# Performance work log

Measured on AMD Instinct MI355X. Metric: run time of the kernel, lower is better.

The kernel has to match this reference:

```python
import jax, jax.numpy as jnp
import numpy as np

B, C, OUT, K, H, W = 16, 128, 128, 3, 128, 128
EPS = 1e-5


def setup_inputs() -> dict:
    key = jax.random.key(0)
    ks = jax.random.split(key, 16)
    s = 0.05  # weight init scale to keep activations tame
    d = {
        "ir_feat": jax.random.normal(ks[0], (B, C, H, W), jnp.float32),
        "vi_feat": jax.random.normal(ks[1], (B, C, H, W), jnp.float32),
        # kernel_gen: 1x1 convs on pooled [B,2C,1,1] -> matmuls
        "kg_w1": jax.random.normal(ks[2], (C // 2, 2 * C), jnp.float32) * s,
        "kg_b1": jax.random.normal(ks[3], (C // 2,), jnp.float32) * s,
        "kg_w2": jax.random.normal(ks[4], (OUT * C * K * K, C // 2), jnp.float32) * s,
        "kg_b2": jax.random.normal(ks[5], (OUT * C * K * K,), jnp.float32) * s,
        # bias_gen
        "bg_w1": jax.random.normal(ks[6], (C // 4, 2 * C), jnp.float32) * s,
        "bg_b1": jax.random.normal(ks[7], (C // 4,), jnp.float32) * s,
        "bg_w2": jax.random.normal(ks[8], (OUT, C // 4), jnp.float32) * s,
        "bg_b2": jax.random.normal(ks[9], (OUT,), jnp.float32) * s,
        # enhance: 1x1 conv (no bias) + BN (eval-mode running stats)
        "en_w": jax.random.normal(ks[10], (C, 2 * C), jnp.float32) * s,
        "bn_gamma": jnp.ones((C,), jnp.float32),
        "bn_beta": jnp.zeros((C,), jnp.float32),
        "bn_mean": jax.random.normal(ks[11], (C,), jnp.float32) * 0.1,
        "bn_var": jax.random.uniform(ks[12], (C,), jnp.float32, 0.5, 1.5),
    }
    return d


def reference(ir_feat, vi_feat, kg_w1, kg_b1, kg_w2, kg_b2,
              bg_w1, bg_b1, bg_w2, bg_b2, en_w,
              bn_gamma, bn_beta, bn_mean, bn_var):
    concat = jnp.concatenate([ir_feat, vi_feat], axis=1)        # [B,2C,H,W]
    pooled = concat.mean(axis=(2, 3))                            # AdaptiveAvgPool2d(1) -> [B,2C]

    # dynamic kernel generation (1x1 convs on 1x1 spatial == matmuls)
    hk = jax.nn.relu(pooled @ kg_w1.T + kg_b1)                   # [B,C/2]
    dyn_k = (hk @ kg_w2.T + kg_b2).reshape(B, OUT, C, K, K)      # per-sample conv weights
    hb = jax.nn.relu(pooled @ bg_w1.T + bg_b1)                   # [B,C/4]
    dyn_b = hb @ bg_w2.T + bg_b2                                 # [B,OUT]

    # enhance: 1x1 conv -> BN(eval) -> ReLU
    enh = jnp.einsum('bchw,oc->bohw', concat, en_w)              # [B,C,H,W]
    inv = (bn_gamma / jnp.sqrt(bn_var + EPS))[:, None, None]
    enh = jax.nn.relu(enh * inv + (bn_beta - bn_mean * bn_gamma / jnp.sqrt(bn_var + EPS))[:, None, None])

    # per-sample dynamic conv2d, batched via vmap (replaces the python loop)
    def conv_one(x, w, b):  # x:[C,H,W], w:[OUT,C,K,K], b:[OUT]
        y = jax.lax.conv_general_dilated(
            x[None], w, window_strides=(1, 1), padding=[(1, 1), (1, 1)],
            dimension_numbers=('NCHW', 'OIHW', 'NCHW'))[0]
        return y + b[:, None, None]

    return jax.vmap(conv_one)(enh, dyn_k, dyn_b)                 # [B,OUT,H,W]
```

## Files before the change

### kernel.cpp

```cpp
#include <hip/hip_runtime.h>
#include <hip/hip_bf16.h>

#define B_    16
#define C_    128
#define TWOC  256
#define OUT_  128
#define HW    16384
#define WDIM  128
#define HDIM  128
#define KTOT  1152

typedef __attribute__((ext_vector_type(8))) short short8;
typedef __attribute__((ext_vector_type(4))) float floatx4;

__device__ __forceinline__ ushort f2bf(float f) {
    union { float f; uint u; } x; x.f = f;
    uint r = (x.u + 0x7FFFu + ((x.u >> 16) & 1u)) >> 16;
    return (ushort)r;
}
__device__ __forceinline__ float bf2f(ushort u) {
    union { float f; uint u; } x; x.u = ((uint)u) << 16;
    return x.f;
}

__global__ __launch_bounds__(256) void zero_pooled_kernel(float* __restrict__ p) {
    int i = blockIdx.x * 256 + threadIdx.x;
    if (i < B_ * TWOC) p[i] = 0.f;
}

__global__ __launch_bounds__(256) void enhance_kernel(
    const float* __restrict__ ir, const float* __restrict__ vi,
    const float* __restrict__ en_w,
    const float* __restrict__ gamma, const float* __restrict__ beta,
    const float* __restrict__ mean, const float* __restrict__ var,
    ushort* __restrict__ enh, float* __restrict__ pooled)
{
    __shared__ ushort Xs[128][40];
    __shared__ float red[256];
    int b = blockIdx.y;
    int p0 = blockIdx.x * 128;
    int t = threadIdx.x;
    int lane = t & 63, wave = t >> 6;
    int wr = wave >> 1, wc = wave & 1;
    int lr = lane & 15, kg = lane >> 4;
    int px = t & 127, half = t >> 7;

    floatx4 acc[4][4] = {};
    float pp[8];

    #pragma unroll
    for (int kc = 0; kc < 8; ++kc) {
        int c2b = kc * 32 + half * 16;
        const float* src = (c2b < C_) ? (ir + ((size_t)b * C_ + c2b) * HW + p0 + px)
                                      : (vi + ((size_t)b * C_ + (c2b - C_)) * HW + p0 + px);
        uint u[8];
        #pragma unroll
        for (int jj = 0; jj < 8; ++jj) {
            float f0 = src[(size_t)(2 * jj) * HW];
            float f1 = src[(size_t)(2 * jj + 1) * HW];
            u[jj] = (uint)f2bf(f0) | ((uint)f2bf(f1) << 16);
        }
        __syncthreads();
        uint4* dst = (uint4*)&Xs[px][half * 16];
        dst[0] = make_uint4(u[0], u[1], u[2], u[3]);
        dst[1] = make_uint4(u[4], u[5], u[6], u[7]);
        __syncthreads();

        short8 af[4], bfr[4];
        #pragma unroll
        for (int i2 = 0; i2 < 4; ++i2) {
            int co = wr * 64 + i2 * 16 + lr;
            const float* wp = en_w + (size_t)co * TWOC + kc * 32 + kg * 8;
            float4 w0 = *(const float4*)wp;
            float4 w1 = *(const float4*)(wp + 4);
            short8 a;
            a[0] = (short)f2bf(w0.x); a[1] = (short)f2bf(w0.y);
            a[2] = (short)f2bf(w0.z); a[3] = (short)f2bf(w0.w);
            a[4] = (short)f2bf(w1.x); a[5] = (short)f2bf(w1.y);
            a[6] = (short)f2bf(w1.z); a[7] = (short)f2bf(w1.w);
            af[i2] = a;
        }
        #pragma unroll
        for (int j = 0; j < 4; ++j) {
            int pl = wc * 64 + j * 16 + lr;
            bfr[j] = *(const short8*)&Xs[pl][kg * 8];
        }
        #pragma unroll
        for (int i2 = 0; i2 < 4; ++i2)
            #pragma unroll
            for (int j = 0; j < 4; ++j)
                acc[i2][j] = __builtin_amdgcn_mfma_f32_16x16x32_bf16(af[i2], bfr[j], acc[i2][j], 0, 0, 0);

        {
            int c = t & 31, grp = t >> 5;
            float s = 0.f;
            #pragma unroll
            for (int q = 0; q < 16; ++q) s += bf2f(Xs[grp * 16 + q][c]);
            pp[kc] = s;
        }
    }

    #pragma unroll
    for (int i2 = 0; i2 < 4; ++i2) {
        int co_b = wr * 64 + i2 * 16 + kg * 4;
        float4 g  = *(const float4*)&gamma[co_b];
        float4 vv = *(const float4*)&var[co_b];
        float4 bt = *(const float4*)&beta[co_b];
        float4 mn = *(const float4*)&mean[co_b];
        float inv0 = g.x * rsqrtf(vv.x + 1e-5f), inv1 = g.y * rsqrtf(vv.y + 1e-5f);
        float inv2 = g.z * rsqrtf(vv.z + 1e-5f), inv3 = g.w * rsqrtf(vv.w + 1e-5f);
        float ad0 = bt.x - mn.x * inv0, ad1 = bt.y - mn.y * inv1;
        float ad2 = bt.z - mn.z * inv2, ad3 = bt.w - mn.w * inv3;
        #pragma unroll
        for (int j = 0; j < 4; ++j) {
            int pl = wc * 64 + j * 16 + lr;
            float v0 = fmaxf(acc[i2][j][0] * inv0 + ad0, 0.f);
            float v1 = fmaxf(acc[i2][j][1] * inv1 + ad1, 0.f);
            float v2 = fmaxf(acc[i2][j][2] * inv2 + ad2, 0.f);
            float v3 = fmaxf(acc[i2][j][3] * inv3 + ad3, 0.f);
            uint2 pk;
            pk.x = (uint)f2bf(v0) | ((uint)f2bf(v1) << 16);
            pk.y = (uint)f2bf(v2) | ((uint)f2bf(v3) << 16);
            *(uint2*)&enh[((size_t)b * HW + p0 + pl) * C_ + co_b] = pk;
        }
    }

    #pragma unroll
    for (int kc = 0; kc < 8; ++kc) {
        __syncthreads();
        red[t] = pp[kc];
        __syncthreads();
        if (t < 32) {
            float s = red[t] + red[32 + t] + red[64 + t] + red[96 + t]
                    + red[128 + t] + red[160 + t] + red[192 + t] + red[224 + t];
            atomicAdd(&pooled[b * TWOC + kc * 32 + t], s);
        }
    }
}

__global__ __launch_bounds__(256) void gen_mlp1_kernel(
    const float* __restrict__ pooled,
    const float* __restrict__ kg_w1, const float* __restrict__ kg_b1,
    const float* __restrict__ bg_w1, const float* __restrict__ bg_b1,
    float* __restrict__ hk, float* __restrict__ hb)
{
    const float scale = 1.0f / (float)HW;
    int idx = blockIdx.x * 256 + threadIdx.x;
    if (idx < B_ * 64) {
        int b = idx >> 6, j = idx & 63;
        const float4* w = (const float4*)(kg_w1 + (size_t)j * TWOC);
        const float4* p = (const float4*)(pooled + b * TWOC);
        float s = 0.f;
        #pragma unroll 8
        for (int q = 0; q < 64; ++q) {
            float4 wv = w[q], pv = p[q];
            s += (wv.x * pv.x + wv.y * pv.y) + (wv.z * pv.z + wv.w * pv.w);
        }
        hk[idx] = fmaxf(kg_b1[j] + s * scale, 0.f);
    } else if (idx < B_ * 64 + B_ * 32) {
        int e = idx - B_ * 64;
        int b = e >> 5, j = e & 31;
        const float4* w = (const float4*)(bg_w1 + (size_t)j * TWOC);
        const float4* p = (const float4*)(pooled + b * TWOC);
        float s = 0.f;
        #pragma unroll 8
        for (int q = 0; q < 64; ++q) {
            float4 wv = w[q], pv = p[q];
            s += (wv.x * pv.x + wv.y * pv.y) + (wv.z * pv.z + wv.w * pv.w);
        }
        hb[e] = fmaxf(bg_b1[j] + s * scale, 0.f);
    }
}

__global__ __launch_bounds__(256) void gen_dynk_kernel(
    const float* __restrict__ kg_w2, const float* __restrict__ kg_b2,
    const float* __restrict__ hk, const float* __restrict__ hb,
    const float* __restrict__ bg_w2, const float* __restrict__ bg_b2,
    ushort* __restrict__ dynk, float* __restrict__ dyn_b)
{
    __shared__ float hk_s[B_][64];
    int t = threadIdx.x;
    for (int i = t; i < B_ * 64; i += 256) hk_s[i >> 6][i & 63] = hk[i];
    __syncthreads();

    int i = blockIdx.x * 256 + t;
    int kk = i >> 14;
    int o  = (i >> 7) & 127;
    int c  = i & 127;
    int r  = o * KTOT + c * 9 + kk;

    float wrow[64];
    const float4* w4 = (const float4*)(kg_w2 + (size_t)r * 64);
    #pragma unroll
    for (int q = 0; q < 16; ++q) {
        float4 v = w4[q];
        wrow[4 * q + 0] = v.x; wrow[4 * q + 1] = v.y;
        wrow[4 * q + 2] = v.z; wrow[4 * q + 3] = v.w;
    }
    float bias = kg_b2[r];
    #pragma unroll
    for (int b = 0; b < B_; ++b) {
        float s = bias;
        #pragma unroll
        for (int k2 = 0; k2 < 64; ++k2) s += hk_s[b][k2] * wrow[k2];
        dynk[((size_t)(b * 9 + kk) * 128 + o) * 128 + c] = f2bf(s);
    }

    if (blockIdx.x == 0) {
        for (int e = t; e < B_ * OUT_; e += 256) {
            int b = e >> 7, o2 = e & 127;
            float s = bg_b2[o2];
            const float* w = bg_w2 + o2 * 32;
            const float* h = hb + b * 32;
            #pragma unroll
            for (int k2 = 0; k2 < 32; ++k2) s += h[k2] * w[k2];
            dyn_b[e] = s;
        }
    }
}

__global__ __launch_bounds__(256, 3) void dynconv_kernel(
    const ushort* __restrict__ enh, const ushort* __restrict__ dynk,
    const float* __restrict__ dyn_b, float* __restrict__ out)
{
    __shared__ ushort halo[180][72];
    const int b = blockIdx.z;
    const int gy0 = blockIdx.y * 8, gx0 = blockIdx.x * 16;
    const int t = threadIdx.x, lane = t & 63, wave = t >> 6;
    const int wr = wave >> 1, wc = wave & 1;
    const int lr = lane & 15, kg = lane >> 4;
    const ushort* dynk_b = dynk + (size_t)b * 9 * 128 * 128;
    const ushort* enh_b  = enh + (size_t)b * HW * C_;

    floatx4 acc[4][4] = {};
    short8 a_cur[8], a_nxt[8];

    for (int h = 0; h < 2; ++h) {
        uint4 hreg[6];
        #pragma unroll
        for (int s = 0; s < 6; ++s) {
            int seg = s * 256 + t;
            int hp = seg >> 3, c8 = seg & 7;
            uint4 v = make_uint4(0, 0, 0, 0);
            if (hp < 180) {
                int hy = hp / 18, hx = hp - hy * 18;
                int gy = gy0 - 1 + hy, gx = gx0 - 1 + hx;
                if ((unsigned)gy < 128u && (unsigned)gx < 128u)
                    v = *(const uint4*)&enh_b[((size_t)(gy * WDIM + gx)) * C_ + h * 64 + c8 * 8];
            }
            hreg[s] = v;
        }
        #pragma unroll
        for (int q = 0; q < 8; ++q) {
            int ks = q >> 2, i2 = q & 3;
            int o = wr * 64 + i2 * 16 + lr;
            a_cur[q] = *(const short8*)&dynk_b[(size_t)(0 * 128 + o) * 128 + h * 64 + ks * 32 + kg * 8];
        }
        __syncthreads();
        #pragma unroll
        for (int s = 0; s < 6; ++s) {
            int seg = s * 256 + t;
            int hp = seg >> 3, c8 = seg & 7;
            if (hp < 180) *(uint4*)&halo[hp][c8 * 8] = hreg[s];
        }
        __syncthreads();

        #pragma unroll
        for (int kk = 0; kk < 9; ++kk) {
            if (kk < 8) {
                #pragma unroll
                for (int q = 0; q < 8; ++q) {
                    int ks = q >> 2, i2 = q & 3;
                    int o = wr * 64 + i2 * 16 + lr;
                    a_nxt[q] = *(const short8*)&dynk_b[(size_t)((kk + 1) * 128 + o) * 128 + h * 64 + ks * 32 + kg * 8];
                }
            }
            const int kh = kk / 3, kw = kk - kh * 3;
            #pragma unroll
            for (int ks = 0; ks < 2; ++ks) {
                short8 bfr[4];
                #pragma unroll
                for (int j = 0; j < 4; ++j) {
                    int p = wc * 64 + j * 16 + lr;
                    int py = p >> 4, px = p & 15;
                    bfr[j] = *(const short8*)&halo[(py + kh) * 18 + (px + kw)][ks * 32 + kg * 8];
                }
                #pragma unroll
                for (int i2 = 0; i2 < 4; ++i2)
                    #pragma unroll
                    for (int j = 0; j < 4; ++j)
                        acc[i2][j] = __builtin_amdgcn_mfma_f32_16x16x32_bf16(a_cur[ks * 4 + i2], bfr[j], acc[i2][j], 0, 0, 0);
            }
            #pragma unroll
            for (int q = 0; q < 8; ++q) a_cur[q] = a_nxt[q];
        }
    }

    #pragma unroll
    for (int i2 = 0; i2 < 4; ++i2) {
        int o_b = wr * 64 + i2 * 16 + kg * 4;
        float4 db = *(const float4*)&dyn_b[b * OUT_ + o_b];
        float dbv[4] = {db.x, db.y, db.z, db.w};
        #pragma unroll
        for (int j = 0; j < 4; ++j) {
            int p = wc * 64 + j * 16 + lr;
            int py = p >> 4, px = p & 15;
            int gy = gy0 + py, gx = gx0 + px;
            #pragma unroll
            for (int r = 0; r < 4; ++r) {
                int o = o_b + r;
                out[((size_t)(b * OUT_ + o)) * HW + gy * WDIM + gx] = acc[i2][j][r] + dbv[r];
            }
        }
    }
}

extern "C" void kernel_launch(void* const* d_in, const int* in_sizes, int n_in,
                              void* d_out, int out_size, void* d_ws, size_t ws_size,
                              hipStream_t stream)
{
    const float* ir    = (const float*)d_in[0];
    const float* vi    = (const float*)d_in[1];
    const float* kg_w1 = (const float*)d_in[2];
    const float* kg_b1 = (const float*)d_in[3];
    const float* kg_w2 = (const float*)d_in[4];
    const float* kg_b2 = (const float*)d_in[5];
    const float* bg_w1 = (const float*)d_in[6];
    const float* bg_b1 = (const float*)d_in[7];
    const float* bg_w2 = (const float*)d_in[8];
    const float* bg_b2 = (const float*)d_in[9];
    const float* en_w  = (const float*)d_in[10];
    const float* bn_g  = (const float*)d_in[11];
    const float* bn_b  = (const float*)d_in[12];
    const float* bn_m  = (const float*)d_in[13];
    const float* bn_v  = (const float*)d_in[14];
    float* out = (float*)d_out;

    char* ws = (char*)d_ws;
    float*  pooled = (float*)(ws + 0);
    float*  dyn_b  = (float*)(ws + 16384);
    float*  hk     = (float*)(ws + 24576);
    float*  hb     = (float*)(ws + 28672);
    ushort* dynk   = (ushort*)(ws + 32768);
    ushort* enh    = (ushort*)(ws + 32768 + 4718592);

    zero_pooled_kernel<<<16, 256, 0, stream>>>(pooled);
    enhance_kernel<<<dim3(HDIM, B_), 256, 0, stream>>>(ir, vi, en_w, bn_g, bn_b,
                                                       bn_m, bn_v, enh, pooled);
    gen_mlp1_kernel<<<6, 256, 0, stream>>>(pooled, kg_w1, kg_b1, bg_w1, bg_b1, hk, hb);
    gen_dynk_kernel<<<576, 256, 0, stream>>>(kg_w2, kg_b2, hk, hb, bg_w2, bg_b2, dynk, dyn_b);
    dynconv_kernel<<<dim3(WDIM / 16, HDIM / 8, B_), 256, 0, stream>>>(enh, dynk, dyn_b, out);
}
```

Baseline: 694.3 us.

## Prefetch next channel chunk in enhance kernel and pre-convert weights to bf16

The enhance kernel now loads the next chunk of input channels and weights into registers while the current chunk runs its MFMAs, a software-pipelining scheme. A new prep kernel converts en_w to bf16 once and replaces the zero kernel. The pooled reduction is interleaved into the main loop instead of running as a separate tail loop. Packed bf16 conversion uses the v_cvt_pk_bf16_f32 instruction. This raises register pressure, and when the workspace is too small the bf16 weights are parked in the tail of the output buffer, which later gets overwritten by the final kernel.

```diff
diff --git a/kernel.cpp b/kernel.cpp
--- a/kernel.cpp
+++ b/kernel.cpp
@@ -22,64 +22,88 @@
     union { float f; uint u; } x; x.u = ((uint)u) << 16;
     return x.f;
 }
-
-__global__ __launch_bounds__(256) void zero_pooled_kernel(float* __restrict__ p) {
+__device__ __forceinline__ uint cvt_pk_bf16(float lo, float hi) {
+    uint r;
+    asm("v_cvt_pk_bf16_f32 %0, %1, %2" : "=v"(r) : "v"(lo), "v"(hi));
+    return r;
+}
+
+__global__ __launch_bounds__(256) void prep_kernel(
+    const float* __restrict__ en_w, ushort* __restrict__ en_w_bf,
+    float* __restrict__ pooled)
+{
     int i = blockIdx.x * 256 + threadIdx.x;
-    if (i < B_ * TWOC) p[i] = 0.f;
+    en_w_bf[i] = f2bf(en_w[i]);
+    if (i < B_ * TWOC) pooled[i] = 0.f;
 }
 
 __global__ __launch_bounds__(256) void enhance_kernel(
     const float* __restrict__ ir, const float* __restrict__ vi,
-    const float* __restrict__ en_w,
+    const ushort* __restrict__ en_w_bf,
     const float* __restrict__ gamma, const float* __restrict__ beta,
     const float* __restrict__ mean, const float* __restrict__ var,
     ushort* __restrict__ enh, float* __restrict__ pooled)
 {
     __shared__ ushort Xs[128][40];
     __shared__ float red[256];
-    int b = blockIdx.y;
-    int p0 = blockIdx.x * 128;
-    int t = threadIdx.x;
-    int lane = t & 63, wave = t >> 6;
-    int wr = wave >> 1, wc = wave & 1;
-    int lr = lane & 15, kg = lane >> 4;
-    int px = t & 127, half = t >> 7;
+    const int b = blockIdx.y;
+    const int p0 = blockIdx.x * 128;
+    const int t = threadIdx.x;
+    const int lane = t & 63, wave = t >> 6;
+    const int wr = wave >> 1, wc = wave & 1;
+    const int lr = lane & 15, kg = lane >> 4;
+    const int px = t & 127, half = t >> 7;
+    const int pc = t & 31, grp = t >> 5;
 
     floatx4 acc[4][4] = {};
-    float pp[8];
-
-    #pragma unroll
-    for (int kc = 0; kc < 8; ++kc) {
-        int c2b = kc * 32 + half * 16;
-        const float* src = (c2b < C_) ? (ir + ((size_t)b * C_ + c2b) * HW + p0 + px)
-                                      : (vi + ((size_t)b * C_ + (c2b - C_)) * HW + p0 + px);
-        uint u[8];
-        #pragma unroll
-        for (int jj = 0; jj < 8; ++jj) {
-            float f0 = src[(size_t)(2 * jj) * HW];
-            float f1 = src[(size_t)(2 * jj + 1) * HW];
-            u[jj] = (uint)f2bf(f0) | ((uint)f2bf(f1) << 16);
-        }
-        __syncthreads();
-        uint4* dst = (uint4*)&Xs[px][half * 16];
-        dst[0] = make_uint4(u[0], u[1], u[2], u[3]);
-        dst[1] = make_uint4(u[4], u[5], u[6], u[7]);
-        __syncthreads();
-
-        short8 af[4], bfr[4];
+    float fcur[16], fnxt[16];
+    short8 a_cur[4], a_nxt[4];
+
+    {
+        const float* src = ir + ((size_t)b * C_ + half * 16) * HW + p0 + px;
+        #pragma unroll
+        for (int jj = 0; jj < 16; ++jj) fcur[jj] = src[(size_t)jj * HW];
         #pragma unroll
         for (int i2 = 0; i2 < 4; ++i2) {
             int co = wr * 64 + i2 * 16 + lr;
-            const float* wp = en_w + (size_t)co * TWOC + kc * 32 + kg * 8;
-            float4 w0 = *(const float4*)wp;
-            float4 w1 = *(const float4*)(wp + 4);
-            short8 a;
-            a[0] = (short)f2bf(w0.x); a[1] = (short)f2bf(w0.y);
-            a[2] = (short)f2bf(w0.z); a[3] = (short)f2bf(w0.w);
-            a[4] = (short)f2bf(w1.x); a[5] = (short)f2bf(w1.y);
-            a[6] = (short)f2bf(w1.z); a[7] = (short)f2bf(w1.w);
-            af[i2] = a;
-        }
+            a_cur[i2] = *(const short8*)&en_w_bf[(size_t)co * TWOC + kg * 8];
+        }
+    }
+
+    #pragma unroll
+    for (int kc = 0; kc < 8; ++kc) {
+        __syncthreads();
+        {
+            uint u[8];
+            #pragma unroll
+            for (int jj = 0; jj < 8; ++jj)
+                u[jj] = cvt_pk_bf16(fcur[2 * jj], fcur[2 * jj + 1]);
+            uint4* dst = (uint4*)&Xs[px][half * 16];
+            dst[0] = make_uint4(u[0], u[1], u[2], u[3]);
+            dst[1] = make_uint4(u[4], u[5], u[6], u[7]);
+        }
+        if (kc > 0 && t < 32) {
+            float s = red[t] + red[32 + t] + red[64 + t] + red[96 + t]
+                    + red[128 + t] + red[160 + t] + red[192 + t] + red[224 + t];
+            atomicAdd(&pooled[b * TWOC + (kc - 1) * 32 + t], s);
+        }
+        __syncthreads();
+
+        if (kc < 7) {
+            int c2b = (kc + 1) * 32 + half * 16;
+            const float* src = (c2b < C_)
+                ? ir + ((size_t)b * C_ + c2b) * HW + p0 + px
+                : vi + ((size_t)b * C_ + (c2b - C_)) * HW + p0 + px;
+            #pragma unroll
+            for (int jj = 0; jj < 16; ++jj) fnxt[jj] = src[(size_t)jj * HW];
+            #pragma unroll
+            for (int i2 = 0; i2 < 4; ++i2) {
+                int co = wr * 64 + i2 * 16 + lr;
+                a_nxt[i2] = *(const short8*)&en_w_bf[(size_t)co * TWOC + (kc + 1) * 32 + kg * 8];
+            }
+        }
+
+        short8 bfr[4];
         #pragma unroll
         for (int j = 0; j < 4; ++j) {
             int pl = wc * 64 + j * 16 + lr;
@@ -89,15 +113,28 @@
         for (int i2 = 0; i2 < 4; ++i2)
             #pragma unroll
             for (int j = 0; j < 4; ++j)
-                acc[i2][j] = __builtin_amdgcn_mfma_f32_16x16x32_bf16(af[i2], bfr[j], acc[i2][j], 0, 0, 0);
+                acc[i2][j] = __builtin_amdgcn_mfma_f32_16x16x32_bf16(a_cur[i2], bfr[j], acc[i2][j], 0, 0, 0);
 
         {
-            int c = t & 31, grp = t >> 5;
             float s = 0.f;
             #pragma unroll
-            for (int q = 0; q < 16; ++q) s += bf2f(Xs[grp * 16 + q][c]);
-            pp[kc] = s;
-        }
+            for (int q = 0; q < 16; ++q) s += bf2f(Xs[grp * 16 + q][pc]);
+            red[t] = s;
+        }
+
+        if (kc < 7) {
+            #pragma unroll
+            for (int jj = 0; jj < 16; ++jj) fcur[jj] = fnxt[jj];
+            #pragma unroll
+            for (int i2 = 0; i2 < 4; ++i2) a_cur[i2] = a_nxt[i2];
+        }
+    }
+
+    __syncthreads();
+    if (t < 32) {
+        float s = red[t] + red[32 + t] + red[64 + t] + red[96 + t]
+                + red[128 + t] + red[160 + t] + red[192 + t] + red[224 + t];
+        atomicAdd(&pooled[b * TWOC + 7 * 32 + t], s);
     }
 
     #pragma unroll
@@ -119,21 +156,9 @@
             float v2 = fmaxf(acc[i2][j][2] * inv2 + ad2, 0.f);
             float v3 = fmaxf(acc[i2][j][3] * inv3 + ad3, 0.f);
             uint2 pk;
-            pk.x = (uint)f2bf(v0) | ((uint)f2bf(v1) << 16);
-            pk.y = (uint)f2bf(v2) | ((uint)f2bf(v3) << 16);
+            pk.x = cvt_pk_bf16(v0, v1);
+            pk.y = cvt_pk_bf16(v2, v3);
             *(uint2*)&enh[((size_t)b * HW + p0 + pl) * C_ + co_b] = pk;
-        }
-    }
-
-    #pragma unroll
-    for (int kc = 0; kc < 8; ++kc) {
-        __syncthreads();
-        red[t] = pp[kc];
-        __syncthreads();
-        if (t < 32) {
-            float s = red[t] + red[32 + t] + red[64 + t] + red[96 + t]
-                    + red[128 + t] + red[160 + t] + red[192 + t] + red[224 + t];
-            atomicAdd(&pooled[b * TWOC + kc * 32 + t], s);
         }
     }
 }
@@ -344,8 +369,13 @@
     ushort* dynk   = (ushort*)(ws + 32768);
     ushort* enh    = (ushort*)(ws + 32768 + 4718592);
 
-    zero_pooled_kernel<<<16, 256, 0, stream>>>(pooled);
-    enhance_kernel<<<dim3(HDIM, B_), 256, 0, stream>>>(ir, vi, en_w, bn_g, bn_b,
+    size_t en_off = 32768 + 4718592 + 67108864;
+    ushort* en_w_bf = (ws_size >= en_off + 65536)
+                    ? (ushort*)(ws + en_off)
+                    : (ushort*)((char*)d_out + (size_t)out_size - 65536);
+
+    prep_kernel<<<128, 256, 0, stream>>>(en_w, en_w_bf, pooled);
+    enhance_kernel<<<dim3(HDIM, B_), 256, 0, stream>>>(ir, vi, en_w_bf, bn_g, bn_b,
                                                        bn_m, bn_v, enh, pooled);
     gen_mlp1_kernel<<<6, 256, 0, stream>>>(pooled, kg_w1, kg_b1, bg_w1, bg_b1, hk, hb);
     gen_dynk_kernel<<<576, 256, 0, stream>>>(kg_w2, kg_b2, hk, hb, bg_w2, bg_b2, dynk, dyn_b);
```

Result: faster. 590.5 us (-14.9%).
